# Performance work log

Hardware: AMD Instinct MI355X
Metric: run time of the kernel (lower is better)

The kernel has to match this reference:

```python
import jax, jax.numpy as jnp
import numpy as np

B, S, H = 4, 2048, 2048
E, K = 8, 2


def setup_inputs() -> dict:
    key = jax.random.key(0)
    k1, k2, k3 = jax.random.split(key, 3)
    hidden_states = jax.random.normal(k1, (B, S, H), dtype=jnp.float32)
    # torch nn.Linear weight layout: [out_features, in_features]
    gate_w = jax.random.normal(k2, (E, H), dtype=jnp.float32) * (1.0 / np.sqrt(H))
    expert_w = jax.random.normal(k3, (E, H, H), dtype=jnp.float32) * (1.0 / np.sqrt(H))
    return {"hidden_states": hidden_states, "gate_w": gate_w, "expert_w": expert_w}


def reference(hidden_states, gate_w, expert_w):
    b, s, h = hidden_states.shape
    x = hidden_states.reshape(-1, h)                      # [T, H]
    T = x.shape[0]
    router_logits = x @ gate_w.T                          # [T, E]
    probs = jax.nn.softmax(router_logits.astype(jnp.float32), axis=-1)
    topk_w, topk_idx = jax.lax.top_k(probs, K)            # [T, K]
    topk_w = topk_w / jnp.sum(topk_w, axis=-1, keepdims=True)  # norm_topk_prob
    topk_w = topk_w.astype(x.dtype)
    # dense combine weights: cw[t, e] = sum_k topk_w[t, k] * (topk_idx[t, k] == e)
    cw = jnp.zeros((T, E), dtype=x.dtype).at[jnp.arange(T)[:, None], topk_idx].add(topk_w)
    # per-expert outputs: expert e computes x @ W_e^T  (W_e is [out, in])
    expert_out = jnp.einsum('th,edh->ted', x, expert_w)   # [T, E, H]
    out = jnp.einsum('ted,te->td', expert_out, cw)        # [T, H]
    return out.reshape(b, s, h), router_logits
```

## Files before the change

### kernel.cpp

```cpp
#include <hip/hip_runtime.h>
#include <hip/hip_bf16.h>

#define T_TOK 8192
#define H_DIM 2048
#define NE 8

typedef float f32x4 __attribute__((ext_vector_type(4)));
typedef short s16x8 __attribute__((ext_vector_type(8)));

typedef __attribute__((address_space(3))) unsigned int lds_uint;
typedef __attribute__((address_space(1))) const unsigned int glob_uint;

static __device__ __forceinline__ void async_ld16(const void* g, void* l) {
    __builtin_amdgcn_global_load_lds((glob_uint*)g, (lds_uint*)l, 16, 0, 0);
}

static __device__ __forceinline__ unsigned short f32_to_bf16(float f) {
    unsigned int u = __builtin_bit_cast(unsigned int, f);
    unsigned int r = (u + 0x7FFFu + ((u >> 16) & 1u)) >> 16;
    return (unsigned short)r;
}

__global__ __launch_bounds__(256) void prep_kernel(
        const float* __restrict__ w, unsigned short* __restrict__ wb,
        int* __restrict__ cnt) {
    const long g = (long)blockIdx.x * 256 + threadIdx.x;
    if (g < NE) cnt[g] = 0;
    const long nt = (long)gridDim.x * 256;
    const long N_W4 = (long)NE * H_DIM * H_DIM / 4;
    const float4* w4 = (const float4*)w;
    ushort4* wb4 = (ushort4*)wb;
    for (long i = g; i < N_W4; i += nt) {
        float4 v = w4[i];
        wb4[i] = make_ushort4(f32_to_bf16(v.x), f32_to_bf16(v.y),
                              f32_to_bf16(v.z), f32_to_bf16(v.w));
    }
}

__global__ __launch_bounds__(256) void router_kernel(
        const float* __restrict__ x, const float* __restrict__ gate,
        unsigned short* __restrict__ xb, float* __restrict__ logits,
        int* __restrict__ cnt, int* __restrict__ list, float* __restrict__ wl) {
    __shared__ float4 gs[NE * H_DIM / 4];
    __shared__ int aExp[32];
    __shared__ float aW[32];
    const float4* g4 = (const float4*)gate;
    for (int i = threadIdx.x; i < NE * H_DIM / 4; i += 256) gs[i] = g4[i];
    __syncthreads();

    const int wave = threadIdx.x >> 6, lane = threadIdx.x & 63;

    for (int it = 0; it < 4; ++it) {
        const int tok = wave * 4 + it;
        const int t = blockIdx.x * 16 + tok;
        const float4* xr = (const float4*)(x + (long)t * H_DIM);
        ushort4* xw = (ushort4*)(xb + (long)t * H_DIM);
        float acc[NE];
#pragma unroll
        for (int e = 0; e < NE; ++e) acc[e] = 0.f;
#pragma unroll
        for (int i = 0; i < 8; ++i) {
            float4 xv = xr[i * 64 + lane];
            xw[i * 64 + lane] = make_ushort4(f32_to_bf16(xv.x), f32_to_bf16(xv.y),
                                             f32_to_bf16(xv.z), f32_to_bf16(xv.w));
#pragma unroll
            for (int e = 0; e < NE; ++e) {
                float4 gv = gs[e * 512 + i * 64 + lane];
                acc[e] += xv.x * gv.x + xv.y * gv.y + xv.z * gv.z + xv.w * gv.w;
            }
        }
#pragma unroll
        for (int e = 0; e < NE; ++e)
#pragma unroll
            for (int off = 32; off > 0; off >>= 1)
                acc[e] += __shfl_xor(acc[e], off, 64);

        if (lane == 0) {
            float l0 = -1e30f; int i0 = 0;
#pragma unroll
            for (int e = 0; e < NE; ++e)
                if (acc[e] > l0) { l0 = acc[e]; i0 = e; }
            float l1 = -1e30f; int i1 = 0;
#pragma unroll
            for (int e = 0; e < NE; ++e)
                if (e != i0 && acc[e] > l1) { l1 = acc[e]; i1 = e; }
            float e1v = __expf(l1 - l0);
            float inv = 1.f / (1.f + e1v);
#pragma unroll
            for (int e = 0; e < NE; ++e) logits[(long)t * NE + e] = acc[e];
            aExp[tok * 2] = i0;     aW[tok * 2] = inv;
            aExp[tok * 2 + 1] = i1; aW[tok * 2 + 1] = e1v * inv;
        }
    }
    __syncthreads();

    if (threadIdx.x < NE) {
        const int e = threadIdx.x;
        int c = 0;
#pragma unroll
        for (int k = 0; k < 32; ++k) c += (aExp[k] == e);
        if (c) {
            int pos = atomicAdd(&cnt[e], c);
            for (int k = 0; k < 32; ++k)
                if (aExp[k] == e) {
                    list[e * T_TOK + pos] = blockIdx.x * 16 + (k >> 1);
                    wl[e * T_TOK + pos] = aW[k];
                    ++pos;
                }
        }
    }
}

__global__ __launch_bounds__(256, 4) void moe_gemm(
        const unsigned short* __restrict__ xb, const unsigned short* __restrict__ wb,
        const int* __restrict__ cnt, const int* __restrict__ list,
        const float* __restrict__ wl, float* __restrict__ out) {
    __shared__ uint4 As[1024];
    __shared__ uint4 Bs[1024];
    __shared__ int tIdx[128];
    __shared__ float tw[128];

    const int bx = blockIdx.x;
    const int e  = bx >> 10;
    const int rt = (bx >> 4) & 63;
    const int ct = bx & 15;
    const int n = cnt[e];
    const int row0 = rt << 7;
    if (row0 >= n) return;
    const int rv = min(128, n - row0);

    const int tid = threadIdx.x;
    if (tid < 128) {
        if (tid < rv) {
            tIdx[tid] = list[e * T_TOK + row0 + tid];
            tw[tid]   = wl[e * T_TOK + row0 + tid];
        } else { tIdx[tid] = 0; tw[tid] = 0.f; }
    }
    __syncthreads();

    const int wave = tid >> 6, lane = tid & 63;
    const int wm = (wave >> 1) << 6;
    const int wn = (wave & 1) << 6;
    const int quad = lane >> 4, l16 = lane & 15;

    f32x4 acc[4][4];
#pragma unroll
    for (int i = 0; i < 4; ++i)
#pragma unroll
        for (int j = 0; j < 4; ++j) acc[i][j] = (f32x4){0.f, 0.f, 0.f, 0.f};

    const unsigned short* aSrc[4];
    const unsigned short* bSrc[4];
    const long wbase = (long)e * H_DIM * H_DIM + (long)(ct * 128) * H_DIM;
#pragma unroll
    for (int i = 0; i < 4; ++i) {
        const int p = i * 256 + wave * 64 + lane;
        const int r = p >> 3;
        const int c = (p & 7) ^ (r & 7);
        aSrc[i] = xb + (long)tIdx[r] * H_DIM + c * 8;
        bSrc[i] = wb + wbase + (long)r * H_DIM + c * 8;
    }

    for (int kt = 0; kt < H_DIM / 64; ++kt) {
        const int k0 = kt * 64;
#pragma unroll
        for (int i = 0; i < 4; ++i) {
            async_ld16(aSrc[i] + k0, &As[i * 256 + wave * 64]);
            async_ld16(bSrc[i] + k0, &Bs[i * 256 + wave * 64]);
        }
        __syncthreads();
#pragma unroll
        for (int ks = 0; ks < 2; ++ks) {
            s16x8 af[4], bfr[4];
            const int kc = ks * 4 + quad;
#pragma unroll
            for (int i = 0; i < 4; ++i) {
                int r = wm + i * 16 + l16;
                af[i] = ((const s16x8*)As)[(r << 3) | (kc ^ (r & 7))];
            }
#pragma unroll
            for (int j = 0; j < 4; ++j) {
                int d = wn + j * 16 + l16;
                bfr[j] = ((const s16x8*)Bs)[(d << 3) | (kc ^ (d & 7))];
            }
#pragma unroll
            for (int i = 0; i < 4; ++i)
#pragma unroll
                for (int j = 0; j < 4; ++j)
                    acc[i][j] = __builtin_amdgcn_mfma_f32_16x16x32_bf16(
                        af[i], bfr[j], acc[i][j], 0, 0, 0);
        }
        __syncthreads();
    }

    const int colbase = ct * 128 + wn;
#pragma unroll
    for (int i = 0; i < 4; ++i) {
        const int rbase = wm + i * 16 + quad * 4;
#pragma unroll
        for (int jr = 0; jr < 4; ++jr) {
            const int r = rbase + jr;
            if (r < rv) {
                const float wgt = tw[r];
                const long orow = (long)tIdx[r] * H_DIM + colbase;
#pragma unroll
                for (int j = 0; j < 4; ++j)
                    atomicAdd(&out[orow + j * 16 + l16], acc[i][j][jr] * wgt);
            }
        }
    }
}

extern "C" void kernel_launch(void* const* d_in, const int* in_sizes, int n_in,
                              void* d_out, int out_size, void* d_ws, size_t ws_size,
                              hipStream_t stream) {
    (void)in_sizes; (void)n_in; (void)out_size; (void)ws_size;
    const float* x    = (const float*)d_in[0];
    const float* gate = (const float*)d_in[1];
    const float* w    = (const float*)d_in[2];

    float* out    = (float*)d_out;
    float* logits = out + (size_t)T_TOK * H_DIM;

    char* ws = (char*)d_ws;
    unsigned short* xb = (unsigned short*)(ws);
    unsigned short* wb = (unsigned short*)(ws + 33554432);
    int*   cnt  = (int*)(ws + 100663296);
    int*   list = (int*)(ws + 100663328);
    float* wl   = (float*)(ws + 100925472);

    hipMemsetAsync(out, 0, (size_t)T_TOK * H_DIM * sizeof(float), stream);
    prep_kernel<<<2048, 256, 0, stream>>>(w, wb, cnt);
    router_kernel<<<512, 256, 0, stream>>>(x, gate, xb, logits, cnt, list, wl);
    moe_gemm<<<8192, 256, 0, stream>>>(xb, wb, cnt, list, wl, out);
}
```

Before: 484.3 us.

## Replace atomic scatter with bf16 per-slot buffer and combine pass; fuse prep and router

Merges weight conversion and routing into one launch. When workspace is large enough, the GEMM writes each token's weighted expert output as bf16 into a dedicated slot (token, k), and a separate combine kernel sums the two slots into the output. This removes the output memset and fp32 atomics. Blocks are also remapped so each XCD handles a fixed group of experts and column tiles, and the gate weights are read straight from global memory instead of staged in LDS. The cost is an extra combine pass, extra bf16 rounding of the partial outputs, and a dependence on workspace size for which path runs.

```diff
diff --git a/kernel.cpp b/kernel.cpp
--- a/kernel.cpp
+++ b/kernel.cpp
@@ -17,38 +17,39 @@
 
 static __device__ __forceinline__ unsigned short f32_to_bf16(float f) {
     unsigned int u = __builtin_bit_cast(unsigned int, f);
-    unsigned int r = (u + 0x7FFFu + ((u >> 16) & 1u)) >> 16;
-    return (unsigned short)r;
-}
-
-__global__ __launch_bounds__(256) void prep_kernel(
-        const float* __restrict__ w, unsigned short* __restrict__ wb,
-        int* __restrict__ cnt) {
-    const long g = (long)blockIdx.x * 256 + threadIdx.x;
-    if (g < NE) cnt[g] = 0;
-    const long nt = (long)gridDim.x * 256;
-    const long N_W4 = (long)NE * H_DIM * H_DIM / 4;
-    const float4* w4 = (const float4*)w;
-    ushort4* wb4 = (ushort4*)wb;
-    for (long i = g; i < N_W4; i += nt) {
-        float4 v = w4[i];
-        wb4[i] = make_ushort4(f32_to_bf16(v.x), f32_to_bf16(v.y),
-                              f32_to_bf16(v.z), f32_to_bf16(v.w));
-    }
-}
-
-__global__ __launch_bounds__(256) void router_kernel(
+    return (unsigned short)((u + 0x7FFFu + ((u >> 16) & 1u)) >> 16);
+}
+
+static __device__ __forceinline__ float bf2f(unsigned short s) {
+    unsigned int u = ((unsigned int)s) << 16;
+    return __builtin_bit_cast(float, u);
+}
+
+__global__ __launch_bounds__(256) void prep_router(
         const float* __restrict__ x, const float* __restrict__ gate,
-        unsigned short* __restrict__ xb, float* __restrict__ logits,
-        int* __restrict__ cnt, int* __restrict__ list, float* __restrict__ wl) {
-    __shared__ float4 gs[NE * H_DIM / 4];
+        const float* __restrict__ w,
+        unsigned short* __restrict__ xb, unsigned short* __restrict__ wb,
+        float* __restrict__ logits, int* __restrict__ cnt,
+        int* __restrict__ list, float* __restrict__ wl) {
     __shared__ int aExp[32];
     __shared__ float aW[32];
+
+    if (blockIdx.x >= 512) {
+        const long g = (long)(blockIdx.x - 512) * 256 + threadIdx.x;
+        const float4* w4 = (const float4*)w;
+        ushort4* wb4 = (ushort4*)wb;
+#pragma unroll
+        for (int it = 0; it < 16; ++it) {
+            long i = g + (long)it * 524288;
+            float4 v = w4[i];
+            wb4[i] = make_ushort4(f32_to_bf16(v.x), f32_to_bf16(v.y),
+                                  f32_to_bf16(v.z), f32_to_bf16(v.w));
+        }
+        return;
+    }
+
+    const int wave = threadIdx.x >> 6, lane = threadIdx.x & 63;
     const float4* g4 = (const float4*)gate;
-    for (int i = threadIdx.x; i < NE * H_DIM / 4; i += 256) gs[i] = g4[i];
-    __syncthreads();
-
-    const int wave = threadIdx.x >> 6, lane = threadIdx.x & 63;
 
     for (int it = 0; it < 4; ++it) {
         const int tok = wave * 4 + it;
@@ -65,7 +66,7 @@
                                              f32_to_bf16(xv.z), f32_to_bf16(xv.w));
 #pragma unroll
             for (int e = 0; e < NE; ++e) {
-                float4 gv = gs[e * 512 + i * 64 + lane];
+                float4 gv = g4[e * 512 + i * 64 + lane];
                 acc[e] += xv.x * gv.x + xv.y * gv.y + xv.z * gv.z + xv.w * gv.w;
             }
         }
@@ -103,7 +104,7 @@
             int pos = atomicAdd(&cnt[e], c);
             for (int k = 0; k < 32; ++k)
                 if (aExp[k] == e) {
-                    list[e * T_TOK + pos] = blockIdx.x * 16 + (k >> 1);
+                    list[e * T_TOK + pos] = (blockIdx.x * 16 + (k >> 1)) | ((k & 1) << 16);
                     wl[e * T_TOK + pos] = aW[k];
                     ++pos;
                 }
@@ -111,19 +112,25 @@
     }
 }
 
+template<int DENSE>
 __global__ __launch_bounds__(256, 4) void moe_gemm(
         const unsigned short* __restrict__ xb, const unsigned short* __restrict__ wb,
         const int* __restrict__ cnt, const int* __restrict__ list,
-        const float* __restrict__ wl, float* __restrict__ out) {
+        const float* __restrict__ wl, unsigned short* __restrict__ yb,
+        float* __restrict__ out) {
     __shared__ uint4 As[1024];
     __shared__ uint4 Bs[1024];
     __shared__ int tIdx[128];
     __shared__ float tw[128];
 
-    const int bx = blockIdx.x;
-    const int e  = bx >> 10;
-    const int rt = (bx >> 4) & 63;
-    const int ct = bx & 15;
+    const int bx  = blockIdx.x;
+    const int xcd = bx & 7;
+    const int idx = bx >> 3;
+    const int grp = xcd * 16 + (idx & 15);
+    const int rt  = idx >> 4;
+    const int e   = grp >> 4;
+    const int ct  = grp & 15;
+
     const int n = cnt[e];
     const int row0 = rt << 7;
     if (row0 >= n) return;
@@ -157,7 +164,7 @@
         const int p = i * 256 + wave * 64 + lane;
         const int r = p >> 3;
         const int c = (p & 7) ^ (r & 7);
-        aSrc[i] = xb + (long)tIdx[r] * H_DIM + c * 8;
+        aSrc[i] = xb + (long)(tIdx[r] & 0xFFFF) * H_DIM + c * 8;
         bSrc[i] = wb + wbase + (long)r * H_DIM + c * 8;
     }
 
@@ -201,20 +208,49 @@
         for (int jr = 0; jr < 4; ++jr) {
             const int r = rbase + jr;
             if (r < rv) {
+                const int entry = tIdx[r];
                 const float wgt = tw[r];
-                const long orow = (long)tIdx[r] * H_DIM + colbase;
-#pragma unroll
-                for (int j = 0; j < 4; ++j)
-                    atomicAdd(&out[orow + j * 16 + l16], acc[i][j][jr] * wgt);
-            }
-        }
+                if (DENSE) {
+                    const long yrow = ((long)(entry & 0xFFFF) << 1) + (entry >> 16);
+                    unsigned short* yr = yb + yrow * H_DIM + colbase;
+#pragma unroll
+                    for (int j = 0; j < 4; ++j)
+                        yr[j * 16 + l16] = f32_to_bf16(acc[i][j][jr] * wgt);
+                } else {
+                    const long orow = (long)(entry & 0xFFFF) * H_DIM + colbase;
+#pragma unroll
+                    for (int j = 0; j < 4; ++j)
+                        atomicAdd(&out[orow + j * 16 + l16], acc[i][j][jr] * wgt);
+                }
+            }
+        }
+    }
+}
+
+__global__ __launch_bounds__(256) void combine_kernel(
+        const unsigned short* __restrict__ yb, float* __restrict__ out) {
+    const int g = blockIdx.x * 256 + threadIdx.x;
+    float4* out4 = (float4*)out;
+    const ushort4* y4 = (const ushort4*)yb;
+#pragma unroll
+    for (int it = 0; it < 4; ++it) {
+        const int i = g + it * 1048576;
+        const int t = i >> 9, c = i & 511;
+        ushort4 a = y4[(long)(t * 2) * 512 + c];
+        ushort4 b = y4[(long)(t * 2 + 1) * 512 + c];
+        float4 r;
+        r.x = bf2f(a.x) + bf2f(b.x);
+        r.y = bf2f(a.y) + bf2f(b.y);
+        r.z = bf2f(a.z) + bf2f(b.z);
+        r.w = bf2f(a.w) + bf2f(b.w);
+        out4[i] = r;
     }
 }
 
 extern "C" void kernel_launch(void* const* d_in, const int* in_sizes, int n_in,
                               void* d_out, int out_size, void* d_ws, size_t ws_size,
                               hipStream_t stream) {
-    (void)in_sizes; (void)n_in; (void)out_size; (void)ws_size;
+    (void)in_sizes; (void)n_in; (void)out_size;
     const float* x    = (const float*)d_in[0];
     const float* gate = (const float*)d_in[1];
     const float* w    = (const float*)d_in[2];
@@ -225,12 +261,33 @@
     char* ws = (char*)d_ws;
     unsigned short* xb = (unsigned short*)(ws);
     unsigned short* wb = (unsigned short*)(ws + 33554432);
-    int*   cnt  = (int*)(ws + 100663296);
-    int*   list = (int*)(ws + 100663328);
-    float* wl   = (float*)(ws + 100925472);
-
-    hipMemsetAsync(out, 0, (size_t)T_TOK * H_DIM * sizeof(float), stream);
-    prep_kernel<<<2048, 256, 0, stream>>>(w, wb, cnt);
-    router_kernel<<<512, 256, 0, stream>>>(x, gate, xb, logits, cnt, list, wl);
-    moe_gemm<<<8192, 256, 0, stream>>>(xb, wb, cnt, list, wl, out);
-}
+
+    const size_t NEED_DENSE = 168297472;
+    const bool dense = ws_size >= NEED_DENSE;
+
+    unsigned short* yb;
+    int* cnt; int* list; float* wl;
+    if (dense) {
+        yb   = (unsigned short*)(ws + 100663296);
+        cnt  = (int*)(ws + 167772160);
+        list = (int*)(ws + 167773184);
+        wl   = (float*)(ws + 168035328);
+    } else {
+        yb   = nullptr;
+        cnt  = (int*)(ws + 100663296);
+        list = (int*)(ws + 100664320);
+        wl   = (float*)(ws + 100926464);
+    }
+
+    hipMemsetAsync(cnt, 0, NE * sizeof(int), stream);
+    if (!dense)
+        hipMemsetAsync(out, 0, (size_t)T_TOK * H_DIM * sizeof(float), stream);
+
+    prep_router<<<2560, 256, 0, stream>>>(x, gate, w, xb, wb, logits, cnt, list, wl);
+    if (dense) {
+        moe_gemm<1><<<8192, 256, 0, stream>>>(xb, wb, cnt, list, wl, yb, out);
+        combine_kernel<<<4096, 256, 0, stream>>>(yb, out);
+    } else {
+        moe_gemm<0><<<8192, 256, 0, stream>>>(xb, wb, cnt, list, wl, yb, out);
+    }
+}
```

Result: no change. 491.9 us (+1.6%).

## Fuse weight bf16 conversion into GEMM and replace output atomics with combine pass

Applied to the files above, without the earlier changes.

Drops the separate weight-conversion prep kernel and instead loads fp32 expert weights directly in the GEMM, truncating them to bf16 in registers before storing to LDS. Per-slot expert outputs are written as bf16 to a [T,2,H] buffer, and a new combine kernel sums the two slots, replacing fp32 atomicAdd on a zeroed output. Blocks are remapped to group expert/column tiles per XCD for L2 reuse, and occupancy hint drops to 3. This trades extra fp32 weight traffic and synchronous B loads for removing the memset, the prep pass and atomics, and adds truncation and bf16 intermediate rounding error.

```diff
diff --git a/kernel.cpp b/kernel.cpp
--- a/kernel.cpp
+++ b/kernel.cpp
@@ -17,24 +17,21 @@
 
 static __device__ __forceinline__ unsigned short f32_to_bf16(float f) {
     unsigned int u = __builtin_bit_cast(unsigned int, f);
-    unsigned int r = (u + 0x7FFFu + ((u >> 16) & 1u)) >> 16;
-    return (unsigned short)r;
-}
-
-__global__ __launch_bounds__(256) void prep_kernel(
-        const float* __restrict__ w, unsigned short* __restrict__ wb,
-        int* __restrict__ cnt) {
-    const long g = (long)blockIdx.x * 256 + threadIdx.x;
-    if (g < NE) cnt[g] = 0;
-    const long nt = (long)gridDim.x * 256;
-    const long N_W4 = (long)NE * H_DIM * H_DIM / 4;
-    const float4* w4 = (const float4*)w;
-    ushort4* wb4 = (ushort4*)wb;
-    for (long i = g; i < N_W4; i += nt) {
-        float4 v = w4[i];
-        wb4[i] = make_ushort4(f32_to_bf16(v.x), f32_to_bf16(v.y),
-                              f32_to_bf16(v.z), f32_to_bf16(v.w));
-    }
+    return (unsigned short)((u + 0x7FFFu + ((u >> 16) & 1u)) >> 16);
+}
+
+static __device__ __forceinline__ float bf2f(unsigned int hi16) {
+    return __builtin_bit_cast(float, hi16 & 0xFFFF0000u);
+}
+
+static __device__ __forceinline__ unsigned int pack_bf16_trunc(float lo, float hi) {
+#if __has_builtin(__builtin_amdgcn_perm)
+    return __builtin_amdgcn_perm(__builtin_bit_cast(unsigned int, hi),
+                                 __builtin_bit_cast(unsigned int, lo), 0x07060302u);
+#else
+    return (__builtin_bit_cast(unsigned int, lo) >> 16) |
+           (__builtin_bit_cast(unsigned int, hi) & 0xFFFF0000u);
+#endif
 }
 
 __global__ __launch_bounds__(256) void router_kernel(
@@ -103,7 +100,7 @@
             int pos = atomicAdd(&cnt[e], c);
             for (int k = 0; k < 32; ++k)
                 if (aExp[k] == e) {
-                    list[e * T_TOK + pos] = blockIdx.x * 16 + (k >> 1);
+                    list[e * T_TOK + pos] = (blockIdx.x * 16 + (k >> 1)) | ((k & 1) << 16);
                     wl[e * T_TOK + pos] = aW[k];
                     ++pos;
                 }
@@ -111,19 +108,23 @@
     }
 }
 
-__global__ __launch_bounds__(256, 4) void moe_gemm(
-        const unsigned short* __restrict__ xb, const unsigned short* __restrict__ wb,
+__global__ __launch_bounds__(256, 3) void moe_gemm(
+        const unsigned short* __restrict__ xb, const float* __restrict__ wf,
         const int* __restrict__ cnt, const int* __restrict__ list,
-        const float* __restrict__ wl, float* __restrict__ out) {
+        const float* __restrict__ wl, unsigned short* __restrict__ yb) {
     __shared__ uint4 As[1024];
     __shared__ uint4 Bs[1024];
     __shared__ int tIdx[128];
     __shared__ float tw[128];
 
-    const int bx = blockIdx.x;
-    const int e  = bx >> 10;
-    const int rt = (bx >> 4) & 63;
-    const int ct = bx & 15;
+    const int bx  = blockIdx.x;
+    const int xcd = bx & 7;
+    const int idx = bx >> 3;
+    const int grp = ((idx >> 6) << 3) | xcd;
+    const int rt  = idx & 63;
+    const int e   = grp >> 4;
+    const int ct  = grp & 15;
+
     const int n = cnt[e];
     const int row0 = rt << 7;
     if (row0 >= n) return;
@@ -150,23 +151,43 @@
         for (int j = 0; j < 4; ++j) acc[i][j] = (f32x4){0.f, 0.f, 0.f, 0.f};
 
     const unsigned short* aSrc[4];
-    const unsigned short* bSrc[4];
-    const long wbase = (long)e * H_DIM * H_DIM + (long)(ct * 128) * H_DIM;
 #pragma unroll
     for (int i = 0; i < 4; ++i) {
         const int p = i * 256 + wave * 64 + lane;
         const int r = p >> 3;
         const int c = (p & 7) ^ (r & 7);
-        aSrc[i] = xb + (long)tIdx[r] * H_DIM + c * 8;
-        bSrc[i] = wb + wbase + (long)r * H_DIM + c * 8;
+        aSrc[i] = xb + (long)(tIdx[r] & 0xFFFF) * H_DIM + c * 8;
+    }
+    const float4* bSrc4[4];
+    int dstc[4];
+    const long wbase = (long)e * H_DIM * H_DIM + (long)(ct * 128) * H_DIM;
+#pragma unroll
+    for (int i = 0; i < 4; ++i) {
+        const int q = i * 256 + tid;
+        const int r = q >> 3, c = q & 7;
+        bSrc4[i] = (const float4*)(wf + wbase + (long)r * H_DIM + c * 8);
+        dstc[i] = (r << 3) | (c ^ (r & 7));
     }
 
     for (int kt = 0; kt < H_DIM / 64; ++kt) {
         const int k0 = kt * 64;
 #pragma unroll
+        for (int i = 0; i < 4; ++i)
+            async_ld16(aSrc[i] + k0, &As[i * 256 + wave * 64]);
+        float4 b0[4], b1[4];
+#pragma unroll
         for (int i = 0; i < 4; ++i) {
-            async_ld16(aSrc[i] + k0, &As[i * 256 + wave * 64]);
-            async_ld16(bSrc[i] + k0, &Bs[i * 256 + wave * 64]);
+            b0[i] = bSrc4[i][kt * 16];
+            b1[i] = bSrc4[i][kt * 16 + 1];
+        }
+#pragma unroll
+        for (int i = 0; i < 4; ++i) {
+            uint4 d;
+            d.x = pack_bf16_trunc(b0[i].x, b0[i].y);
+            d.y = pack_bf16_trunc(b0[i].z, b0[i].w);
+            d.z = pack_bf16_trunc(b1[i].x, b1[i].y);
+            d.w = pack_bf16_trunc(b1[i].z, b1[i].w);
+            Bs[dstc[i]] = d;
         }
         __syncthreads();
 #pragma unroll
@@ -201,13 +222,40 @@
         for (int jr = 0; jr < 4; ++jr) {
             const int r = rbase + jr;
             if (r < rv) {
+                const int entry = tIdx[r];
                 const float wgt = tw[r];
-                const long orow = (long)tIdx[r] * H_DIM + colbase;
+                const long yrow = ((long)(entry & 0xFFFF) << 1) + (entry >> 16);
+                unsigned short* yr = yb + yrow * H_DIM + colbase;
 #pragma unroll
                 for (int j = 0; j < 4; ++j)
-                    atomicAdd(&out[orow + j * 16 + l16], acc[i][j][jr] * wgt);
-            }
-        }
+                    yr[j * 16 + l16] = f32_to_bf16(acc[i][j][jr] * wgt);
+            }
+        }
+    }
+}
+
+__global__ __launch_bounds__(256) void combine_kernel(
+        const unsigned short* __restrict__ yb, float* __restrict__ out) {
+    const int g = blockIdx.x * 256 + threadIdx.x;
+    const uint4* y4 = (const uint4*)yb;
+    float4* out4 = (float4*)out;
+#pragma unroll
+    for (int it = 0; it < 4; ++it) {
+        const int i = g + it * 524288;
+        const int t = i >> 8, c = i & 255;
+        uint4 a = y4[(long)(t * 2) * 256 + c];
+        uint4 b = y4[(long)(t * 2 + 1) * 256 + c];
+        float4 r0, r1;
+        r0.x = bf2f(a.x << 16) + bf2f(b.x << 16);
+        r0.y = bf2f(a.x)       + bf2f(b.x);
+        r0.z = bf2f(a.y << 16) + bf2f(b.y << 16);
+        r0.w = bf2f(a.y)       + bf2f(b.y);
+        r1.x = bf2f(a.z << 16) + bf2f(b.z << 16);
+        r1.y = bf2f(a.z)       + bf2f(b.z);
+        r1.z = bf2f(a.w << 16) + bf2f(b.w << 16);
+        r1.w = bf2f(a.w)       + bf2f(b.w);
+        out4[(long)i * 2]     = r0;
+        out4[(long)i * 2 + 1] = r1;
     }
 }
 
@@ -224,13 +272,13 @@
 
     char* ws = (char*)d_ws;
     unsigned short* xb = (unsigned short*)(ws);
-    unsigned short* wb = (unsigned short*)(ws + 33554432);
+    unsigned short* yb = (unsigned short*)(ws + 33554432);
     int*   cnt  = (int*)(ws + 100663296);
-    int*   list = (int*)(ws + 100663328);
-    float* wl   = (float*)(ws + 100925472);
-
-    hipMemsetAsync(out, 0, (size_t)T_TOK * H_DIM * sizeof(float), stream);
-    prep_kernel<<<2048, 256, 0, stream>>>(w, wb, cnt);
+    int*   list = (int*)(ws + 100664320);
+    float* wl   = (float*)(ws + 100926464);
+
+    hipMemsetAsync(cnt, 0, NE * sizeof(int), stream);
     router_kernel<<<512, 256, 0, stream>>>(x, gate, xb, logits, cnt, list, wl);
-    moe_gemm<<<8192, 256, 0, stream>>>(xb, wb, cnt, list, wl, out);
-}
+    moe_gemm<<<8192, 256, 0, stream>>>(xb, w, cnt, list, wl, yb);
+    combine_kernel<<<2048, 256, 0, stream>>>(yb, out);
+}
```

After: 493.8 us. About the same (+2.0%).
